# Kernel tuning notes

Measured on AMD Instinct MI355X. Metric: run time of the kernel, lower is better.

Reference implementation:

```python
import jax, jax.numpy as jnp
import numpy as np

T, B, I, H = 2048, 32, 1024, 1024


def setup_inputs() -> dict:
    key = jax.random.key(0)
    k0, k1, k2, k3, k4 = jax.random.split(key, 5)
    s = 1.0 / np.sqrt(H)  # torch RNN-style uniform init scale
    return {
        "x": jax.random.normal(k0, (T, B, I), jnp.float32),
        "h0": jnp.zeros((1, B, H), jnp.float32),
        "w_ih": jax.random.uniform(k1, (3 * H, I), jnp.float32, -s, s),
        "w_hh": jax.random.uniform(k2, (3 * H, H), jnp.float32, -s, s),
        "b_ih": jax.random.uniform(k3, (3 * H,), jnp.float32, -s, s),
        "b_hh": jax.random.uniform(k4, (3 * H,), jnp.float32, -s, s),
    }


def reference(x, h0, w_ih, w_hh, b_ih, b_hh):
    # SMRU1 cell: gates = x@w_ih^T + b_ih + h@w_hh^T + b_hh -> chunk (k,f,a)
    # softmax over the 3 gates per feature; hy = ksm*h + asm
    def step(h, x_t):
        gates = x_t @ w_ih.T + b_ih + h @ w_hh.T + b_hh  # [B, 3H]
        k, f, a = jnp.split(gates, 3, axis=-1)           # each [B, H]
        st = jax.nn.softmax(jnp.stack([k, f, a], axis=-1), axis=-1)  # [B, H, 3]
        hy = st[..., 0] * h + st[..., 2]
        return hy, hy

    h_last, out = jax.lax.scan(step, h0[0], x)  # out: [T, B, H]
    return out
```

## Files before the change

### kernel.cpp

```cpp
#include <hip/hip_runtime.h>
#include <stdint.h>

typedef __bf16 bf16;
typedef __bf16 bf16x8 __attribute__((ext_vector_type(8)));
typedef float f32x4 __attribute__((ext_vector_type(4)));
typedef unsigned int u32x4 __attribute__((ext_vector_type(4)));

#define T_STEPS 2048

static constexpr size_t OFF_XBF  = 0;
static constexpr size_t OFF_WIHB = 134217728;
static constexpr size_t OFF_WR   = 140509184;
static constexpr size_t OFF_GX   = 146800640;
static constexpr size_t OFF_HBUF = 549453824;
static constexpr size_t WS_NEED  = 549584960;

union PK8 { bf16 b[8]; uint4 u; };
union PK4 { bf16 b[4]; uint2 u; };

__global__ void cvt_x_kernel(const float* __restrict__ x, bf16* __restrict__ xb) {
    size_t i = (size_t)blockIdx.x * 256 + threadIdx.x;
    const float4* p = (const float4*)x + i * 2;
    float4 v0 = p[0], v1 = p[1];
    PK8 pk;
    pk.b[0]=(bf16)v0.x; pk.b[1]=(bf16)v0.y; pk.b[2]=(bf16)v0.z; pk.b[3]=(bf16)v0.w;
    pk.b[4]=(bf16)v1.x; pk.b[5]=(bf16)v1.y; pk.b[6]=(bf16)v1.z; pk.b[7]=(bf16)v1.w;
    ((uint4*)xb)[i] = pk.u;
}

__global__ void cvt_w_kernel(const float* __restrict__ wih, const float* __restrict__ whh,
                             const float* __restrict__ h0,
                             bf16* __restrict__ wihb, bf16* __restrict__ wr,
                             bf16* __restrict__ hbuf0) {
    int i = blockIdx.x * 256 + threadIdx.x;
    if (i < 786432) {
        float4 v = ((const float4*)wih)[i];
        PK4 pk;
        pk.b[0]=(bf16)v.x; pk.b[1]=(bf16)v.y; pk.b[2]=(bf16)v.z; pk.b[3]=(bf16)v.w;
        ((uint2*)wihb)[i] = pk.u;
    } else if (i < 1572864) {
        int d = (i - 786432) * 4;
        int g = d / 49152;
        int rem = d - g * 49152;
        int jr = rem >> 10, kk = rem & 1023;
        int srow = (jr >> 4) * 1024 + g * 16 + (jr & 15);
        float4 v = *(const float4*)(whh + (size_t)srow * 1024 + kk);
        PK4 pk;
        pk.b[0]=(bf16)v.x; pk.b[1]=(bf16)v.y; pk.b[2]=(bf16)v.z; pk.b[3]=(bf16)v.w;
        *(uint2*)(wr + d) = pk.u;
    } else {
        int j = (i - 1572864) * 4;
        float4 v = *(const float4*)(h0 + j);
        PK4 pk;
        pk.b[0]=(bf16)v.x; pk.b[1]=(bf16)v.y; pk.b[2]=(bf16)v.z; pk.b[3]=(bf16)v.w;
        *(uint2*)(hbuf0 + j) = pk.u;
    }
}

__global__ __launch_bounds__(256) void gemm_x_kernel(
        const bf16* __restrict__ A, const bf16* __restrict__ W,
        const float* __restrict__ bih, const float* __restrict__ bhh,
        bf16* __restrict__ gx) {
    __shared__ bf16 a_s[128 * 40];
    __shared__ bf16 b_s[128 * 40];
    const int tid = threadIdx.x;
    const int wave = tid >> 6, lane = tid & 63;
    const int wm = wave & 1, wn = wave >> 1;
    const int col = lane & 15, row0 = (lane >> 4) << 2, kq = (lane >> 4) << 3;
    const int m0 = blockIdx.x * 128, n0 = blockIdx.y * 128;
    const int r0 = tid >> 2, c0 = (tid & 3) << 3;
    const int r1 = r0 + 64;
    f32x4 acc[4][4];
    #pragma unroll
    for (int mi = 0; mi < 4; ++mi)
        #pragma unroll
        for (int ni = 0; ni < 4; ++ni) {
            acc[mi][ni][0] = 0.f; acc[mi][ni][1] = 0.f;
            acc[mi][ni][2] = 0.f; acc[mi][ni][3] = 0.f;
        }
    for (int kt = 0; kt < 32; ++kt) {
        const int k0 = kt * 32;
        uint4 va0 = *(const uint4*)(A + (size_t)(m0 + r0) * 1024 + k0 + c0);
        uint4 vb0 = *(const uint4*)(W + (size_t)(n0 + r0) * 1024 + k0 + c0);
        uint4 va1 = *(const uint4*)(A + (size_t)(m0 + r1) * 1024 + k0 + c0);
        uint4 vb1 = *(const uint4*)(W + (size_t)(n0 + r1) * 1024 + k0 + c0);
        __syncthreads();
        *(uint4*)(a_s + r0 * 40 + c0) = va0;
        *(uint4*)(b_s + r0 * 40 + c0) = vb0;
        *(uint4*)(a_s + r1 * 40 + c0) = va1;
        *(uint4*)(b_s + r1 * 40 + c0) = vb1;
        __syncthreads();
        bf16x8 af[4], bfv[4];
        #pragma unroll
        for (int i = 0; i < 4; ++i)
            af[i] = *(const bf16x8*)(a_s + (wm * 64 + i * 16 + col) * 40 + kq);
        #pragma unroll
        for (int i = 0; i < 4; ++i)
            bfv[i] = *(const bf16x8*)(b_s + (wn * 64 + i * 16 + col) * 40 + kq);
        #pragma unroll
        for (int mi = 0; mi < 4; ++mi)
            #pragma unroll
            for (int ni = 0; ni < 4; ++ni)
                acc[mi][ni] = __builtin_amdgcn_mfma_f32_16x16x32_bf16(af[mi], bfv[ni], acc[mi][ni], 0, 0, 0);
    }
    #pragma unroll
    for (int mi = 0; mi < 4; ++mi) {
        const int mbase = m0 + wm * 64 + mi * 16;
        const int t = mbase >> 5;
        const int b0 = (mbase & 31) + row0;
        #pragma unroll
        for (int ni = 0; ni < 4; ++ni) {
            const int n = n0 + wn * 64 + ni * 16 + col;
            const int gt = n >> 10, ii = n & 1023;
            const float bias = bih[n] + bhh[n];
            const size_t off = (((size_t)t * 64 + (ii >> 4)) * 48 + gt * 16 + (ii & 15)) * 32 + b0;
            f32x4 v = acc[mi][ni];
            PK4 pk;
            pk.b[0]=(bf16)(v[0]+bias); pk.b[1]=(bf16)(v[1]+bias);
            pk.b[2]=(bf16)(v[2]+bias); pk.b[3]=(bf16)(v[3]+bias);
            *(uint2*)(gx + off) = pk.u;
        }
    }
}

__global__ __launch_bounds__(384, 1) void smru_rec_kernel(
        const bf16* __restrict__ wr, const bf16* __restrict__ gx,
        const float* __restrict__ h0,
        bf16* __restrict__ hbuf, float* __restrict__ out,
        unsigned int* __restrict__ flags) {
    extern __shared__ char smem[];
    bf16* h_s = (bf16*)smem;
    float* g_s = (float*)(smem + 65536);
    const int g = blockIdx.x;
    const int tid = threadIdx.x;
    const int wave = tid >> 6, lane = tid & 63;
    const int mtile = wave & 1, ntile = wave >> 1;
    const int col = lane & 15, row0 = (lane >> 4) << 2, kq = (lane >> 4) << 3;
    const int f0 = g << 4;

    bf16x8 wreg[32];
    {
        const bf16* wrow = wr + (size_t)g * 49152 + (size_t)(ntile * 16 + col) * 1024 + kq;
        #pragma unroll
        for (int c2 = 0; c2 < 2; ++c2)
            #pragma unroll
            for (int kk = 0; kk < 16; ++kk)
                wreg[c2 * 16 + kk] = *(const bf16x8*)(wrow + c2 * 512 + kk * 32);
    }

    const int b1 = tid >> 4, il1 = tid & 15;
    const int b2 = 24 + (tid >> 4);
    float h1 = h0[b1 * 1024 + f0 + il1];
    float h2 = (tid < 128) ? h0[b2 * 1024 + f0 + il1] : 0.f;

    const int hrow = mtile * 16 + col;
    const int hswz = (hrow & 7) * 8;

    uint2 gv = *(const uint2*)(gx + (((size_t)0 * 64 + g) * 48 + ntile * 16 + col) * 32
                               + mtile * 16 + row0);

    for (int t = 0; t < T_STEPS; ++t) {
        const bf16* hsrc = hbuf + (t & 1) * 32768;
        bf16* hdst = hbuf + ((t + 1) & 1) * 32768;

        u32x4 st0[6];
        #pragma unroll
        for (int j = 0; j < 6; ++j) {
            int s = tid + 384 * j;
            if (j < 5 || tid < 128) {
                int r = s >> 6, c8 = (s & 63) << 3;
                const bf16* p = hsrc + r * 1024 + c8;
                asm volatile("global_load_dwordx4 %0, %1, off sc0 sc1"
                             : "=v"(st0[j]) : "v"(p) : "memory");
            }
        }
        asm volatile("s_waitcnt vmcnt(0)" ::: "memory");
        __builtin_amdgcn_sched_barrier(0);
        #pragma unroll
        for (int j = 0; j < 6; ++j) {
            int s = tid + 384 * j;
            if (j < 5 || tid < 128) {
                int r = s >> 6, c8 = (s & 63) << 3;
                *(u32x4*)(h_s + r * 512 + (c8 ^ ((r & 7) * 8))) = st0[j];
            }
        }
        __syncthreads();

        f32x4 acc, acc2;
        {
            union { uint2 u; bf16 b[4]; } pk; pk.u = gv;
            acc[0] = (float)pk.b[0]; acc[1] = (float)pk.b[1];
            acc[2] = (float)pk.b[2]; acc[3] = (float)pk.b[3];
            acc2[0] = 0.f; acc2[1] = 0.f; acc2[2] = 0.f; acc2[3] = 0.f;
        }

        u32x4 st1[6];
        #pragma unroll
        for (int j = 0; j < 6; ++j) {
            int s = tid + 384 * j;
            if (j < 5 || tid < 128) {
                int r = s >> 6, c8 = (s & 63) << 3;
                const bf16* p = hsrc + r * 1024 + 512 + c8;
                asm volatile("global_load_dwordx4 %0, %1, off sc0 sc1"
                             : "=v"(st1[j]) : "v"(p) : "memory");
            }
        }

        const bf16* hb0 = h_s + hrow * 512;
        #pragma unroll
        for (int kk = 0; kk < 8; ++kk) {
            bf16x8 a0 = *(const bf16x8*)(hb0 + ((kk * 32 + kq) ^ hswz));
            bf16x8 a1 = *(const bf16x8*)(hb0 + (((kk + 8) * 32 + kq) ^ hswz));
            acc  = __builtin_amdgcn_mfma_f32_16x16x32_bf16(a0, wreg[kk], acc, 0, 0, 0);
            acc2 = __builtin_amdgcn_mfma_f32_16x16x32_bf16(a1, wreg[kk + 8], acc2, 0, 0, 0);
        }

        asm volatile("s_waitcnt vmcnt(0)" ::: "memory");
        __builtin_amdgcn_sched_barrier(0);
        #pragma unroll
        for (int j = 0; j < 6; ++j) {
            int s = tid + 384 * j;
            if (j < 5 || tid < 128) {
                int r = s >> 6, c8 = (s & 63) << 3;
                *(u32x4*)(h_s + 16384 + r * 512 + (c8 ^ ((r & 7) * 8))) = st1[j];
            }
        }
        __syncthreads();

        uint2 gvn;
        {
            int tn = (t + 1 < T_STEPS) ? t + 1 : t;
            gvn = *(const uint2*)(gx + (((size_t)tn * 64 + g) * 48 + ntile * 16 + col) * 32
                                  + mtile * 16 + row0);
        }

        const bf16* hb1 = h_s + 16384 + hrow * 512;
        #pragma unroll
        for (int kk = 0; kk < 8; ++kk) {
            bf16x8 a0 = *(const bf16x8*)(hb1 + ((kk * 32 + kq) ^ hswz));
            bf16x8 a1 = *(const bf16x8*)(hb1 + (((kk + 8) * 32 + kq) ^ hswz));
            acc  = __builtin_amdgcn_mfma_f32_16x16x32_bf16(a0, wreg[16 + kk], acc, 0, 0, 0);
            acc2 = __builtin_amdgcn_mfma_f32_16x16x32_bf16(a1, wreg[24 + kk], acc2, 0, 0, 0);
        }

        float* gw = g_s + (ntile * 2 + mtile) * 272;
        gw[(row0 + 0) * 17 + col] = acc[0] + acc2[0];
        gw[(row0 + 1) * 17 + col] = acc[1] + acc2[1];
        gw[(row0 + 2) * 17 + col] = acc[2] + acc2[2];
        gw[(row0 + 3) * 17 + col] = acc[3] + acc2[3];
        __syncthreads();

        float hy1, hy2 = 0.f;
        {
            const int mt = b1 >> 4, rw = b1 & 15;
            const float gk = g_s[(0 + mt) * 272 + rw * 17 + il1];
            const float gf = g_s[(2 + mt) * 272 + rw * 17 + il1];
            const float ga = g_s[(4 + mt) * 272 + rw * 17 + il1];
            const float mx = fmaxf(gk, fmaxf(gf, ga));
            const float ek = __expf(gk - mx), ef = __expf(gf - mx), ea = __expf(ga - mx);
            const float inv = 1.0f / (ek + ef + ea);
            hy1 = ek * inv * h1 + ea * inv;
            h1 = hy1;
        }
        {
            union { bf16 h; unsigned short u; } cv; cv.h = (bf16)hy1;
            unsigned int nb = __shfl_down((unsigned int)cv.u, 1);
            if ((il1 & 1) == 0)
                __hip_atomic_store((unsigned int*)(hdst + b1 * 1024 + f0 + il1),
                                   (unsigned int)cv.u | (nb << 16),
                                   __ATOMIC_RELAXED, __HIP_MEMORY_SCOPE_AGENT);
        }
        if (tid < 128) {
            const int mt = b2 >> 4, rw = b2 & 15;
            const float gk = g_s[(0 + mt) * 272 + rw * 17 + il1];
            const float gf = g_s[(2 + mt) * 272 + rw * 17 + il1];
            const float ga = g_s[(4 + mt) * 272 + rw * 17 + il1];
            const float mx = fmaxf(gk, fmaxf(gf, ga));
            const float ek = __expf(gk - mx), ef = __expf(gf - mx), ea = __expf(ga - mx);
            const float inv = 1.0f / (ek + ef + ea);
            hy2 = ek * inv * h2 + ea * inv;
            h2 = hy2;
            union { bf16 h; unsigned short u; } cv2; cv2.h = (bf16)hy2;
            unsigned int nb2 = __shfl_down((unsigned int)cv2.u, 1);
            if ((il1 & 1) == 0)
                __hip_atomic_store((unsigned int*)(hdst + b2 * 1024 + f0 + il1),
                                   (unsigned int)cv2.u | (nb2 << 16),
                                   __ATOMIC_RELAXED, __HIP_MEMORY_SCOPE_AGENT);
        }

        asm volatile("s_waitcnt vmcnt(0)" ::: "memory");
        __syncthreads();
        if (tid == 0)
            __hip_atomic_store(flags + g, (unsigned int)(t + 1),
                               __ATOMIC_RELAXED, __HIP_MEMORY_SCOPE_AGENT);

        out[((size_t)t * 32 + b1) * 1024 + f0 + il1] = hy1;
        if (tid < 128) out[((size_t)t * 32 + b2) * 1024 + f0 + il1] = hy2;

        gv = gvn;

        if (t + 1 < T_STEPS) {
            const unsigned int tgt = (unsigned int)(t + 1);
            if (tid < 64) {
                for (;;) {
                    unsigned int f = __hip_atomic_load(flags + tid,
                        __ATOMIC_RELAXED, __HIP_MEMORY_SCOPE_AGENT);
                    if (__all((int)(f >= tgt))) break;
                }
            }
            __syncthreads();
            asm volatile("" ::: "memory");
        }
    }
}

extern "C" void kernel_launch(void* const* d_in, const int* in_sizes, int n_in,
                              void* d_out, int out_size, void* d_ws, size_t ws_size,
                              hipStream_t stream) {
    const float* x   = (const float*)d_in[0];
    const float* h0  = (const float*)d_in[1];
    const float* wih = (const float*)d_in[2];
    const float* whh = (const float*)d_in[3];
    const float* bih = (const float*)d_in[4];
    const float* bhh = (const float*)d_in[5];
    float* out = (float*)d_out;
    char* ws = (char*)d_ws;
    if (ws_size < WS_NEED) return;

    bf16* xb   = (bf16*)(ws + OFF_XBF);
    bf16* wihb = (bf16*)(ws + OFF_WIHB);
    bf16* wrp  = (bf16*)(ws + OFF_WR);
    bf16* gx   = (bf16*)(ws + OFF_GX);
    bf16* hbuf = (bf16*)(ws + OFF_HBUF);
    unsigned int* flags = (unsigned int*)(ws + OFF_XBF);

    cvt_x_kernel<<<32768, 256, 0, stream>>>(x, xb);
    cvt_w_kernel<<<6176, 256, 0, stream>>>(wih, whh, h0, wihb, wrp, hbuf);
    gemm_x_kernel<<<dim3(512, 24), 256, 0, stream>>>(xb, wihb, bih, bhh, gx);
    hipMemsetAsync(flags, 0, 256, stream);
    hipFuncSetAttribute((const void*)smru_rec_kernel,
                        hipFuncAttributeMaxDynamicSharedMemorySize, 72064);
    smru_rec_kernel<<<64, 384, 72064, stream>>>(wrp, gx, h0, hbuf, out, flags);
}
```

Before: 9.939 ms.

## Replace per-step flag barrier with tagged hidden-state words polled directly

The recurrent kernel no longer publishes per-block flags and spins on them. Each hidden value is now stored as a 32-bit word that packs the bf16 value with the step index as a tag. Consumers poll the hidden buffer itself, reloading chunks until every tag matches the current step. This removes a full barrier round-trip and a separate flag write and read per timestep, and t=0 loads h0 directly. The cost is twice the bytes per hidden-state load and retry loops, and the buffer reuses the w_ih bf16 region after the input GEMM.

```diff
diff --git a/kernel.cpp b/kernel.cpp
--- a/kernel.cpp
+++ b/kernel.cpp
@@ -5,6 +5,7 @@
 typedef __bf16 bf16x8 __attribute__((ext_vector_type(8)));
 typedef float f32x4 __attribute__((ext_vector_type(4)));
 typedef unsigned int u32x4 __attribute__((ext_vector_type(4)));
+typedef unsigned int u32x2 __attribute__((ext_vector_type(2)));
 
 #define T_STEPS 2048
 
@@ -12,7 +13,6 @@
 static constexpr size_t OFF_WIHB = 134217728;
 static constexpr size_t OFF_WR   = 140509184;
 static constexpr size_t OFF_GX   = 146800640;
-static constexpr size_t OFF_HBUF = 549453824;
 static constexpr size_t WS_NEED  = 549584960;
 
 union PK8 { bf16 b[8]; uint4 u; };
@@ -29,16 +29,14 @@
 }
 
 __global__ void cvt_w_kernel(const float* __restrict__ wih, const float* __restrict__ whh,
-                             const float* __restrict__ h0,
-                             bf16* __restrict__ wihb, bf16* __restrict__ wr,
-                             bf16* __restrict__ hbuf0) {
+                             bf16* __restrict__ wihb, bf16* __restrict__ wr) {
     int i = blockIdx.x * 256 + threadIdx.x;
     if (i < 786432) {
         float4 v = ((const float4*)wih)[i];
         PK4 pk;
         pk.b[0]=(bf16)v.x; pk.b[1]=(bf16)v.y; pk.b[2]=(bf16)v.z; pk.b[3]=(bf16)v.w;
         ((uint2*)wihb)[i] = pk.u;
-    } else if (i < 1572864) {
+    } else {
         int d = (i - 786432) * 4;
         int g = d / 49152;
         int rem = d - g * 49152;
@@ -48,12 +46,6 @@
         PK4 pk;
         pk.b[0]=(bf16)v.x; pk.b[1]=(bf16)v.y; pk.b[2]=(bf16)v.z; pk.b[3]=(bf16)v.w;
         *(uint2*)(wr + d) = pk.u;
-    } else {
-        int j = (i - 1572864) * 4;
-        float4 v = *(const float4*)(h0 + j);
-        PK4 pk;
-        pk.b[0]=(bf16)v.x; pk.b[1]=(bf16)v.y; pk.b[2]=(bf16)v.z; pk.b[3]=(bf16)v.w;
-        *(uint2*)(hbuf0 + j) = pk.u;
     }
 }
 
@@ -126,8 +118,7 @@
 __global__ __launch_bounds__(384, 1) void smru_rec_kernel(
         const bf16* __restrict__ wr, const bf16* __restrict__ gx,
         const float* __restrict__ h0,
-        bf16* __restrict__ hbuf, float* __restrict__ out,
-        unsigned int* __restrict__ flags) {
+        unsigned int* __restrict__ hbt, float* __restrict__ out) {
     extern __shared__ char smem[];
     bf16* h_s = (bf16*)smem;
     float* g_s = (float*)(smem + 65536);
@@ -160,30 +151,85 @@
                                + mtile * 16 + row0);
 
     for (int t = 0; t < T_STEPS; ++t) {
-        const bf16* hsrc = hbuf + (t & 1) * 32768;
-        bf16* hdst = hbuf + ((t + 1) & 1) * 32768;
-
-        u32x4 st0[6];
-        #pragma unroll
-        for (int j = 0; j < 6; ++j) {
-            int s = tid + 384 * j;
-            if (j < 5 || tid < 128) {
-                int r = s >> 6, c8 = (s & 63) << 3;
-                const bf16* p = hsrc + r * 1024 + c8;
-                asm volatile("global_load_dwordx4 %0, %1, off sc0 sc1"
-                             : "=v"(st0[j]) : "v"(p) : "memory");
-            }
-        }
-        asm volatile("s_waitcnt vmcnt(0)" ::: "memory");
-        __builtin_amdgcn_sched_barrier(0);
-        #pragma unroll
-        for (int j = 0; j < 6; ++j) {
-            int s = tid + 384 * j;
-            if (j < 5 || tid < 128) {
-                int r = s >> 6, c8 = (s & 63) << 3;
-                *(u32x4*)(h_s + r * 512 + (c8 ^ ((r & 7) * 8))) = st0[j];
-            }
-        }
+        if (t == 0) {
+            #pragma unroll
+            for (int j = 0; j < 11; ++j) {
+                if (j < 10 || tid < 256) {
+                    int s = tid + 384 * j;
+                    int r = s >> 7, c8 = (s & 127) << 3;
+                    float4 f0v = *(const float4*)(h0 + r * 1024 + c8);
+                    float4 f1v = *(const float4*)(h0 + r * 1024 + c8 + 4);
+                    PK8 pk;
+                    pk.b[0]=(bf16)f0v.x; pk.b[1]=(bf16)f0v.y; pk.b[2]=(bf16)f0v.z; pk.b[3]=(bf16)f0v.w;
+                    pk.b[4]=(bf16)f1v.x; pk.b[5]=(bf16)f1v.y; pk.b[6]=(bf16)f1v.z; pk.b[7]=(bf16)f1v.w;
+                    int hf = c8 >> 9, cc = c8 & 511;
+                    *(uint4*)(h_s + hf * 16384 + r * 512 + (cc ^ ((r & 7) * 8))) = pk.u;
+                }
+            }
+        } else {
+            const unsigned int tag = (unsigned int)t;
+            const unsigned int TT  = tag | (tag << 16);
+            const unsigned int* src = hbt + (size_t)(t & 1) * 32768;
+            u32x4 La[11], Lb[11];
+            unsigned int todo = (tid < 256) ? 0x7FFu : 0x3FFu;
+            #pragma unroll
+            for (int j = 0; j < 11; ++j) {
+                if (j < 10 || tid < 256) {
+                    int s = tid + 384 * j;
+                    int r = s >> 7, c8 = (s & 127) << 3;
+                    const unsigned int* p = src + r * 1024 + c8;
+                    asm volatile("global_load_dwordx4 %0, %2, off sc0 sc1\n\t"
+                                 "global_load_dwordx4 %1, %2, off offset:16 sc0 sc1"
+                                 : "=v"(La[j]), "=v"(Lb[j]) : "v"(p) : "memory");
+                }
+            }
+            for (;;) {
+                asm volatile("s_waitcnt vmcnt(0)" ::: "memory");
+                __builtin_amdgcn_sched_barrier(0);
+                #pragma unroll
+                for (int j = 0; j < 11; ++j) {
+                    if (todo & (1u << j)) {
+                        unsigned int p0 = __builtin_amdgcn_perm(La[j][1], La[j][0], 0x05040100u) ^ TT;
+                        unsigned int p1 = __builtin_amdgcn_perm(La[j][3], La[j][2], 0x05040100u) ^ TT;
+                        unsigned int p2 = __builtin_amdgcn_perm(Lb[j][1], Lb[j][0], 0x05040100u) ^ TT;
+                        unsigned int p3 = __builtin_amdgcn_perm(Lb[j][3], Lb[j][2], 0x05040100u) ^ TT;
+                        if (((p0 | p1) | (p2 | p3)) == 0u) {
+                            todo &= ~(1u << j);
+                        } else {
+                            int s = tid + 384 * j;
+                            int r = s >> 7, c8 = (s & 127) << 3;
+                            const unsigned int* p = src + r * 1024 + c8;
+                            asm volatile("global_load_dwordx4 %0, %2, off sc0 sc1\n\t"
+                                         "global_load_dwordx4 %1, %2, off offset:16 sc0 sc1"
+                                         : "=v"(La[j]), "=v"(Lb[j]) : "v"(p) : "memory");
+                        }
+                    }
+                }
+                if (!__any((int)todo)) break;
+            }
+            #pragma unroll
+            for (int j = 0; j < 11; ++j) {
+                if (j < 10 || tid < 256) {
+                    int s = tid + 384 * j;
+                    int r = s >> 7, c8 = (s & 127) << 3;
+                    uint4 w;
+                    w.x = (La[j][0] >> 16) | (La[j][1] & 0xFFFF0000u);
+                    w.y = (La[j][2] >> 16) | (La[j][3] & 0xFFFF0000u);
+                    w.z = (Lb[j][0] >> 16) | (Lb[j][1] & 0xFFFF0000u);
+                    w.w = (Lb[j][2] >> 16) | (Lb[j][3] & 0xFFFF0000u);
+                    int hf = c8 >> 9, cc = c8 & 511;
+                    *(uint4*)(h_s + hf * 16384 + r * 512 + (cc ^ ((r & 7) * 8))) = w;
+                }
+            }
+        }
+
+        uint2 gvn;
+        {
+            int tn = (t + 1 < T_STEPS) ? t + 1 : t;
+            gvn = *(const uint2*)(gx + (((size_t)tn * 64 + g) * 48 + ntile * 16 + col) * 32
+                                  + mtile * 16 + row0);
+        }
+
         __syncthreads();
 
         f32x4 acc, acc2;
@@ -194,19 +240,8 @@
             acc2[0] = 0.f; acc2[1] = 0.f; acc2[2] = 0.f; acc2[3] = 0.f;
         }
 
-        u32x4 st1[6];
-        #pragma unroll
-        for (int j = 0; j < 6; ++j) {
-            int s = tid + 384 * j;
-            if (j < 5 || tid < 128) {
-                int r = s >> 6, c8 = (s & 63) << 3;
-                const bf16* p = hsrc + r * 1024 + 512 + c8;
-                asm volatile("global_load_dwordx4 %0, %1, off sc0 sc1"
-                             : "=v"(st1[j]) : "v"(p) : "memory");
-            }
-        }
-
         const bf16* hb0 = h_s + hrow * 512;
+        const bf16* hb1 = h_s + 16384 + hrow * 512;
         #pragma unroll
         for (int kk = 0; kk < 8; ++kk) {
             bf16x8 a0 = *(const bf16x8*)(hb0 + ((kk * 32 + kq) ^ hswz));
@@ -214,27 +249,6 @@
             acc  = __builtin_amdgcn_mfma_f32_16x16x32_bf16(a0, wreg[kk], acc, 0, 0, 0);
             acc2 = __builtin_amdgcn_mfma_f32_16x16x32_bf16(a1, wreg[kk + 8], acc2, 0, 0, 0);
         }
-
-        asm volatile("s_waitcnt vmcnt(0)" ::: "memory");
-        __builtin_amdgcn_sched_barrier(0);
-        #pragma unroll
-        for (int j = 0; j < 6; ++j) {
-            int s = tid + 384 * j;
-            if (j < 5 || tid < 128) {
-                int r = s >> 6, c8 = (s & 63) << 3;
-                *(u32x4*)(h_s + 16384 + r * 512 + (c8 ^ ((r & 7) * 8))) = st1[j];
-            }
-        }
-        __syncthreads();
-
-        uint2 gvn;
-        {
-            int tn = (t + 1 < T_STEPS) ? t + 1 : t;
-            gvn = *(const uint2*)(gx + (((size_t)tn * 64 + g) * 48 + ntile * 16 + col) * 32
-                                  + mtile * 16 + row0);
-        }
-
-        const bf16* hb1 = h_s + 16384 + hrow * 512;
         #pragma unroll
         for (int kk = 0; kk < 8; ++kk) {
             bf16x8 a0 = *(const bf16x8*)(hb1 + ((kk * 32 + kq) ^ hswz));
@@ -250,6 +264,8 @@
         gw[(row0 + 3) * 17 + col] = acc[3] + acc2[3];
         __syncthreads();
 
+        const unsigned int ptag = (unsigned int)(t + 1);
+        unsigned int* dstp = hbt + (size_t)((t + 1) & 1) * 32768;
         float hy1, hy2 = 0.f;
         {
             const int mt = b1 >> 4, rw = b1 & 15;
@@ -264,11 +280,14 @@
         }
         {
             union { bf16 h; unsigned short u; } cv; cv.h = (bf16)hy1;
-            unsigned int nb = __shfl_down((unsigned int)cv.u, 1);
-            if ((il1 & 1) == 0)
-                __hip_atomic_store((unsigned int*)(hdst + b1 * 1024 + f0 + il1),
-                                   (unsigned int)cv.u | (nb << 16),
-                                   __ATOMIC_RELAXED, __HIP_MEMORY_SCOPE_AGENT);
+            unsigned int my = ((unsigned int)cv.u << 16) | ptag;
+            unsigned int nb = __shfl_down(my, 1);
+            if ((il1 & 1) == 0) {
+                unsigned int* p = dstp + b1 * 1024 + f0 + il1;
+                u32x2 val; val[0] = my; val[1] = nb;
+                asm volatile("global_store_dwordx2 %0, %1, off sc0 sc1"
+                             :: "v"(p), "v"(val) : "memory");
+            }
         }
         if (tid < 128) {
             const int mt = b2 >> 4, rw = b2 & 15;
@@ -281,36 +300,20 @@
             hy2 = ek * inv * h2 + ea * inv;
             h2 = hy2;
             union { bf16 h; unsigned short u; } cv2; cv2.h = (bf16)hy2;
-            unsigned int nb2 = __shfl_down((unsigned int)cv2.u, 1);
-            if ((il1 & 1) == 0)
-                __hip_atomic_store((unsigned int*)(hdst + b2 * 1024 + f0 + il1),
-                                   (unsigned int)cv2.u | (nb2 << 16),
-                                   __ATOMIC_RELAXED, __HIP_MEMORY_SCOPE_AGENT);
-        }
-
-        asm volatile("s_waitcnt vmcnt(0)" ::: "memory");
-        __syncthreads();
-        if (tid == 0)
-            __hip_atomic_store(flags + g, (unsigned int)(t + 1),
-                               __ATOMIC_RELAXED, __HIP_MEMORY_SCOPE_AGENT);
+            unsigned int my2 = ((unsigned int)cv2.u << 16) | ptag;
+            unsigned int nb2 = __shfl_down(my2, 1);
+            if ((il1 & 1) == 0) {
+                unsigned int* p = dstp + b2 * 1024 + f0 + il1;
+                u32x2 val2; val2[0] = my2; val2[1] = nb2;
+                asm volatile("global_store_dwordx2 %0, %1, off sc0 sc1"
+                             :: "v"(p), "v"(val2) : "memory");
+            }
+        }
 
         out[((size_t)t * 32 + b1) * 1024 + f0 + il1] = hy1;
         if (tid < 128) out[((size_t)t * 32 + b2) * 1024 + f0 + il1] = hy2;
 
         gv = gvn;
-
-        if (t + 1 < T_STEPS) {
-            const unsigned int tgt = (unsigned int)(t + 1);
-            if (tid < 64) {
-                for (;;) {
-                    unsigned int f = __hip_atomic_load(flags + tid,
-                        __ATOMIC_RELAXED, __HIP_MEMORY_SCOPE_AGENT);
-                    if (__all((int)(f >= tgt))) break;
-                }
-            }
-            __syncthreads();
-            asm volatile("" ::: "memory");
-        }
     }
 }
 
@@ -331,14 +334,13 @@
     bf16* wihb = (bf16*)(ws + OFF_WIHB);
     bf16* wrp  = (bf16*)(ws + OFF_WR);
     bf16* gx   = (bf16*)(ws + OFF_GX);
-    bf16* hbuf = (bf16*)(ws + OFF_HBUF);
-    unsigned int* flags = (unsigned int*)(ws + OFF_XBF);
+    unsigned int* hbt = (unsigned int*)(ws + OFF_WIHB);
 
     cvt_x_kernel<<<32768, 256, 0, stream>>>(x, xb);
-    cvt_w_kernel<<<6176, 256, 0, stream>>>(wih, whh, h0, wihb, wrp, hbuf);
+    cvt_w_kernel<<<6144, 256, 0, stream>>>(wih, whh, wihb, wrp);
     gemm_x_kernel<<<dim3(512, 24), 256, 0, stream>>>(xb, wihb, bih, bhh, gx);
-    hipMemsetAsync(flags, 0, 256, stream);
+    hipMemsetAsync(hbt, 0xFF, 262144, stream);
     hipFuncSetAttribute((const void*)smru_rec_kernel,
                         hipFuncAttributeMaxDynamicSharedMemorySize, 72064);
-    smru_rec_kernel<<<64, 384, 72064, stream>>>(wrp, gx, h0, hbuf, out, flags);
-}
+    smru_rec_kernel<<<64, 384, 72064, stream>>>(wrp, gx, h0, hbt, out);
+}
```

New measurement: 18.53 ms. 1.86x slower.

## Merge feature groups into 32 larger recurrent blocks to halve grid-sync participants

Applied to the files above, without the earlier changes.

Each block of the persistent recurrent kernel now covers two 16-feature groups with 768 threads, so 32 blocks synchronise per step instead of 64. This reduces flag polling and the total redundant global reads of h per step. The h loads are issued all at once before the MFMA loop instead of half being overlapped with compute. The first step reads h0 directly, so the h0 conversion pass is dropped and hbuf moves into the dead w_ih bf16 region. In exchange, each block has more threads and uses more shared memory and registers.

```diff
diff --git a/kernel.cpp b/kernel.cpp
--- a/kernel.cpp
+++ b/kernel.cpp
@@ -12,7 +12,6 @@
 static constexpr size_t OFF_WIHB = 134217728;
 static constexpr size_t OFF_WR   = 140509184;
 static constexpr size_t OFF_GX   = 146800640;
-static constexpr size_t OFF_HBUF = 549453824;
 static constexpr size_t WS_NEED  = 549584960;
 
 union PK8 { bf16 b[8]; uint4 u; };
@@ -29,16 +28,14 @@
 }
 
 __global__ void cvt_w_kernel(const float* __restrict__ wih, const float* __restrict__ whh,
-                             const float* __restrict__ h0,
-                             bf16* __restrict__ wihb, bf16* __restrict__ wr,
-                             bf16* __restrict__ hbuf0) {
+                             bf16* __restrict__ wihb, bf16* __restrict__ wr) {
     int i = blockIdx.x * 256 + threadIdx.x;
     if (i < 786432) {
         float4 v = ((const float4*)wih)[i];
         PK4 pk;
         pk.b[0]=(bf16)v.x; pk.b[1]=(bf16)v.y; pk.b[2]=(bf16)v.z; pk.b[3]=(bf16)v.w;
         ((uint2*)wihb)[i] = pk.u;
-    } else if (i < 1572864) {
+    } else {
         int d = (i - 786432) * 4;
         int g = d / 49152;
         int rem = d - g * 49152;
@@ -48,12 +45,6 @@
         PK4 pk;
         pk.b[0]=(bf16)v.x; pk.b[1]=(bf16)v.y; pk.b[2]=(bf16)v.z; pk.b[3]=(bf16)v.w;
         *(uint2*)(wr + d) = pk.u;
-    } else {
-        int j = (i - 1572864) * 4;
-        float4 v = *(const float4*)(h0 + j);
-        PK4 pk;
-        pk.b[0]=(bf16)v.x; pk.b[1]=(bf16)v.y; pk.b[2]=(bf16)v.z; pk.b[3]=(bf16)v.w;
-        *(uint2*)(hbuf0 + j) = pk.u;
     }
 }
 
@@ -123,7 +114,7 @@
     }
 }
 
-__global__ __launch_bounds__(384, 1) void smru_rec_kernel(
+__global__ __launch_bounds__(768, 1) void smru_rec_kernel(
         const bf16* __restrict__ wr, const bf16* __restrict__ gx,
         const float* __restrict__ h0,
         bf16* __restrict__ hbuf, float* __restrict__ out,
@@ -131,16 +122,18 @@
     extern __shared__ char smem[];
     bf16* h_s = (bf16*)smem;
     float* g_s = (float*)(smem + 65536);
-    const int g = blockIdx.x;
+    const int g2 = blockIdx.x;
     const int tid = threadIdx.x;
     const int wave = tid >> 6, lane = tid & 63;
     const int mtile = wave & 1, ntile = wave >> 1;
+    const int glocal = ntile / 3, gate = ntile % 3;
+    const int g = g2 * 2 + glocal;
     const int col = lane & 15, row0 = (lane >> 4) << 2, kq = (lane >> 4) << 3;
-    const int f0 = g << 4;
+    const int f0 = g2 << 5;
 
     bf16x8 wreg[32];
     {
-        const bf16* wrow = wr + (size_t)g * 49152 + (size_t)(ntile * 16 + col) * 1024 + kq;
+        const bf16* wrow = wr + (size_t)g * 49152 + (size_t)(gate * 16 + col) * 1024 + kq;
         #pragma unroll
         for (int c2 = 0; c2 < 2; ++c2)
             #pragma unroll
@@ -148,42 +141,77 @@
                 wreg[c2 * 16 + kk] = *(const bf16x8*)(wrow + c2 * 512 + kk * 32);
     }
 
-    const int b1 = tid >> 4, il1 = tid & 15;
-    const int b2 = 24 + (tid >> 4);
-    float h1 = h0[b1 * 1024 + f0 + il1];
-    float h2 = (tid < 128) ? h0[b2 * 1024 + f0 + il1] : 0.f;
+    const int il = tid & 31;
+    const int b1 = tid >> 5;
+    const int b2 = 24 + (tid >> 5);
+    float h1 = h0[b1 * 1024 + f0 + il];
+    float h2 = (tid < 256) ? h0[b2 * 1024 + f0 + il] : 0.f;
 
     const int hrow = mtile * 16 + col;
     const int hswz = (hrow & 7) * 8;
 
-    uint2 gv = *(const uint2*)(gx + (((size_t)0 * 64 + g) * 48 + ntile * 16 + col) * 32
+    uint2 gv = *(const uint2*)(gx + (((size_t)0 * 64 + g) * 48 + gate * 16 + col) * 32
                                + mtile * 16 + row0);
 
     for (int t = 0; t < T_STEPS; ++t) {
-        const bf16* hsrc = hbuf + (t & 1) * 32768;
-        bf16* hdst = hbuf + ((t + 1) & 1) * 32768;
-
-        u32x4 st0[6];
-        #pragma unroll
-        for (int j = 0; j < 6; ++j) {
-            int s = tid + 384 * j;
-            if (j < 5 || tid < 128) {
-                int r = s >> 6, c8 = (s & 63) << 3;
-                const bf16* p = hsrc + r * 1024 + c8;
-                asm volatile("global_load_dwordx4 %0, %1, off sc0 sc1"
-                             : "=v"(st0[j]) : "v"(p) : "memory");
-            }
-        }
-        asm volatile("s_waitcnt vmcnt(0)" ::: "memory");
-        __builtin_amdgcn_sched_barrier(0);
-        #pragma unroll
-        for (int j = 0; j < 6; ++j) {
-            int s = tid + 384 * j;
-            if (j < 5 || tid < 128) {
-                int r = s >> 6, c8 = (s & 63) << 3;
-                *(u32x4*)(h_s + r * 512 + (c8 ^ ((r & 7) * 8))) = st0[j];
-            }
-        }
+        if (t == 0) {
+            #pragma unroll
+            for (int j = 0; j < 6; ++j) {
+                if (j < 5 || tid < 256) {
+                    int s = tid + 768 * j;
+                    int r = s >> 7, c8 = (s & 127) << 3;
+                    float4 f0v = *(const float4*)(h0 + r * 1024 + c8);
+                    float4 f1v = *(const float4*)(h0 + r * 1024 + c8 + 4);
+                    PK8 pk;
+                    pk.b[0]=(bf16)f0v.x; pk.b[1]=(bf16)f0v.y; pk.b[2]=(bf16)f0v.z; pk.b[3]=(bf16)f0v.w;
+                    pk.b[4]=(bf16)f1v.x; pk.b[5]=(bf16)f1v.y; pk.b[6]=(bf16)f1v.z; pk.b[7]=(bf16)f1v.w;
+                    int hf = c8 >> 9, cc = c8 & 511;
+                    *(uint4*)(h_s + hf * 16384 + r * 512 + (cc ^ ((r & 7) * 8))) = pk.u;
+                }
+            }
+        } else {
+            const bf16* hsrc = hbuf + (size_t)(t & 1) * 32768;
+            u32x4 L0[3], L1[3];
+            #pragma unroll
+            for (int j = 0; j < 3; ++j) {
+                if (j < 2 || tid < 512) {
+                    int s = tid + 768 * j;
+                    int r = s >> 6, c8 = (s & 63) << 3;
+                    const bf16* p = hsrc + r * 1024 + c8;
+                    asm volatile("global_load_dwordx4 %0, %1, off sc0 sc1"
+                                 : "=v"(L0[j]) : "v"(p) : "memory");
+                }
+            }
+            #pragma unroll
+            for (int j = 0; j < 3; ++j) {
+                if (j < 2 || tid < 512) {
+                    int s = tid + 768 * j;
+                    int r = s >> 6, c8 = (s & 63) << 3;
+                    const bf16* p = hsrc + r * 1024 + 512 + c8;
+                    asm volatile("global_load_dwordx4 %0, %1, off sc0 sc1"
+                                 : "=v"(L1[j]) : "v"(p) : "memory");
+                }
+            }
+            asm volatile("s_waitcnt vmcnt(0)" ::: "memory");
+            __builtin_amdgcn_sched_barrier(0);
+            #pragma unroll
+            for (int j = 0; j < 3; ++j) {
+                if (j < 2 || tid < 512) {
+                    int s = tid + 768 * j;
+                    int r = s >> 6, c8 = (s & 63) << 3;
+                    *(u32x4*)(h_s + r * 512 + (c8 ^ ((r & 7) * 8))) = L0[j];
+                    *(u32x4*)(h_s + 16384 + r * 512 + (c8 ^ ((r & 7) * 8))) = L1[j];
+                }
+            }
+        }
+
+        uint2 gvn;
+        {
+            int tn = (t + 1 < T_STEPS) ? t + 1 : t;
+            gvn = *(const uint2*)(gx + (((size_t)tn * 64 + g) * 48 + gate * 16 + col) * 32
+                                  + mtile * 16 + row0);
+        }
+
         __syncthreads();
 
         f32x4 acc, acc2;
@@ -194,19 +222,8 @@
             acc2[0] = 0.f; acc2[1] = 0.f; acc2[2] = 0.f; acc2[3] = 0.f;
         }
 
-        u32x4 st1[6];
-        #pragma unroll
-        for (int j = 0; j < 6; ++j) {
-            int s = tid + 384 * j;
-            if (j < 5 || tid < 128) {
-                int r = s >> 6, c8 = (s & 63) << 3;
-                const bf16* p = hsrc + r * 1024 + 512 + c8;
-                asm volatile("global_load_dwordx4 %0, %1, off sc0 sc1"
-                             : "=v"(st1[j]) : "v"(p) : "memory");
-            }
-        }
-
         const bf16* hb0 = h_s + hrow * 512;
+        const bf16* hb1 = h_s + 16384 + hrow * 512;
         #pragma unroll
         for (int kk = 0; kk < 8; ++kk) {
             bf16x8 a0 = *(const bf16x8*)(hb0 + ((kk * 32 + kq) ^ hswz));
@@ -214,27 +231,6 @@
             acc  = __builtin_amdgcn_mfma_f32_16x16x32_bf16(a0, wreg[kk], acc, 0, 0, 0);
             acc2 = __builtin_amdgcn_mfma_f32_16x16x32_bf16(a1, wreg[kk + 8], acc2, 0, 0, 0);
         }
-
-        asm volatile("s_waitcnt vmcnt(0)" ::: "memory");
-        __builtin_amdgcn_sched_barrier(0);
-        #pragma unroll
-        for (int j = 0; j < 6; ++j) {
-            int s = tid + 384 * j;
-            if (j < 5 || tid < 128) {
-                int r = s >> 6, c8 = (s & 63) << 3;
-                *(u32x4*)(h_s + 16384 + r * 512 + (c8 ^ ((r & 7) * 8))) = st1[j];
-            }
-        }
-        __syncthreads();
-
-        uint2 gvn;
-        {
-            int tn = (t + 1 < T_STEPS) ? t + 1 : t;
-            gvn = *(const uint2*)(gx + (((size_t)tn * 64 + g) * 48 + ntile * 16 + col) * 32
-                                  + mtile * 16 + row0);
-        }
-
-        const bf16* hb1 = h_s + 16384 + hrow * 512;
         #pragma unroll
         for (int kk = 0; kk < 8; ++kk) {
             bf16x8 a0 = *(const bf16x8*)(hb1 + ((kk * 32 + kq) ^ hswz));
@@ -250,12 +246,15 @@
         gw[(row0 + 3) * 17 + col] = acc[3] + acc2[3];
         __syncthreads();
 
+        bf16* hdst = hbuf + (size_t)((t + 1) & 1) * 32768;
+        const int gb = (il >> 4) * 6;
+        const int ic = il & 15;
         float hy1, hy2 = 0.f;
         {
             const int mt = b1 >> 4, rw = b1 & 15;
-            const float gk = g_s[(0 + mt) * 272 + rw * 17 + il1];
-            const float gf = g_s[(2 + mt) * 272 + rw * 17 + il1];
-            const float ga = g_s[(4 + mt) * 272 + rw * 17 + il1];
+            const float gk = g_s[(gb + 0 + mt) * 272 + rw * 17 + ic];
+            const float gf = g_s[(gb + 2 + mt) * 272 + rw * 17 + ic];
+            const float ga = g_s[(gb + 4 + mt) * 272 + rw * 17 + ic];
             const float mx = fmaxf(gk, fmaxf(gf, ga));
             const float ek = __expf(gk - mx), ef = __expf(gf - mx), ea = __expf(ga - mx);
             const float inv = 1.0f / (ek + ef + ea);
@@ -265,16 +264,16 @@
         {
             union { bf16 h; unsigned short u; } cv; cv.h = (bf16)hy1;
             unsigned int nb = __shfl_down((unsigned int)cv.u, 1);
-            if ((il1 & 1) == 0)
-                __hip_atomic_store((unsigned int*)(hdst + b1 * 1024 + f0 + il1),
+            if ((il & 1) == 0)
+                __hip_atomic_store((unsigned int*)(hdst + b1 * 1024 + f0 + il),
                                    (unsigned int)cv.u | (nb << 16),
                                    __ATOMIC_RELAXED, __HIP_MEMORY_SCOPE_AGENT);
         }
-        if (tid < 128) {
+        if (tid < 256) {
             const int mt = b2 >> 4, rw = b2 & 15;
-            const float gk = g_s[(0 + mt) * 272 + rw * 17 + il1];
-            const float gf = g_s[(2 + mt) * 272 + rw * 17 + il1];
-            const float ga = g_s[(4 + mt) * 272 + rw * 17 + il1];
+            const float gk = g_s[(gb + 0 + mt) * 272 + rw * 17 + ic];
+            const float gf = g_s[(gb + 2 + mt) * 272 + rw * 17 + ic];
+            const float ga = g_s[(gb + 4 + mt) * 272 + rw * 17 + ic];
             const float mx = fmaxf(gk, fmaxf(gf, ga));
             const float ek = __expf(gk - mx), ef = __expf(gf - mx), ea = __expf(ga - mx);
             const float inv = 1.0f / (ek + ef + ea);
@@ -282,8 +281,8 @@
             h2 = hy2;
             union { bf16 h; unsigned short u; } cv2; cv2.h = (bf16)hy2;
             unsigned int nb2 = __shfl_down((unsigned int)cv2.u, 1);
-            if ((il1 & 1) == 0)
-                __hip_atomic_store((unsigned int*)(hdst + b2 * 1024 + f0 + il1),
+            if ((il & 1) == 0)
+                __hip_atomic_store((unsigned int*)(hdst + b2 * 1024 + f0 + il),
                                    (unsigned int)cv2.u | (nb2 << 16),
                                    __ATOMIC_RELAXED, __HIP_MEMORY_SCOPE_AGENT);
         }
@@ -291,11 +290,11 @@
         asm volatile("s_waitcnt vmcnt(0)" ::: "memory");
         __syncthreads();
         if (tid == 0)
-            __hip_atomic_store(flags + g, (unsigned int)(t + 1),
+            __hip_atomic_store(flags + g2, (unsigned int)(t + 1),
                                __ATOMIC_RELAXED, __HIP_MEMORY_SCOPE_AGENT);
 
-        out[((size_t)t * 32 + b1) * 1024 + f0 + il1] = hy1;
-        if (tid < 128) out[((size_t)t * 32 + b2) * 1024 + f0 + il1] = hy2;
+        out[((size_t)t * 32 + b1) * 1024 + f0 + il] = hy1;
+        if (tid < 256) out[((size_t)t * 32 + b2) * 1024 + f0 + il] = hy2;
 
         gv = gvn;
 
@@ -303,7 +302,7 @@
             const unsigned int tgt = (unsigned int)(t + 1);
             if (tid < 64) {
                 for (;;) {
-                    unsigned int f = __hip_atomic_load(flags + tid,
+                    unsigned int f = __hip_atomic_load(flags + (tid & 31),
                         __ATOMIC_RELAXED, __HIP_MEMORY_SCOPE_AGENT);
                     if (__all((int)(f >= tgt))) break;
                 }
@@ -331,14 +330,14 @@
     bf16* wihb = (bf16*)(ws + OFF_WIHB);
     bf16* wrp  = (bf16*)(ws + OFF_WR);
     bf16* gx   = (bf16*)(ws + OFF_GX);
-    bf16* hbuf = (bf16*)(ws + OFF_HBUF);
+    bf16* hbuf = (bf16*)(ws + OFF_WIHB);
     unsigned int* flags = (unsigned int*)(ws + OFF_XBF);
 
     cvt_x_kernel<<<32768, 256, 0, stream>>>(x, xb);
-    cvt_w_kernel<<<6176, 256, 0, stream>>>(wih, whh, h0, wihb, wrp, hbuf);
+    cvt_w_kernel<<<6144, 256, 0, stream>>>(wih, whh, wihb, wrp);
     gemm_x_kernel<<<dim3(512, 24), 256, 0, stream>>>(xb, wihb, bih, bhh, gx);
-    hipMemsetAsync(flags, 0, 256, stream);
+    hipMemsetAsync(flags, 0, 128, stream);
     hipFuncSetAttribute((const void*)smru_rec_kernel,
-                        hipFuncAttributeMaxDynamicSharedMemorySize, 72064);
-    smru_rec_kernel<<<64, 384, 72064, stream>>>(wrp, gx, h0, hbuf, out, flags);
-}
+                        hipFuncAttributeMaxDynamicSharedMemorySize, 78592);
+    smru_rec_kernel<<<32, 768, 78592, stream>>>(wrp, gx, h0, hbuf, out, flags);
+}
```

After: 21.00 ms. +111.3%, slower.
